# Kernel optimization log

Hardware: AMD Instinct MI355X
Metric: run time of the kernel (lower is better)

Reference implementation:

```python
import jax, jax.numpy as jnp
import numpy as np

N, E, D, H = 50000, 400000, 64, 2  # nodes, edges, model_dim, heads


def setup_inputs() -> dict:
    key = jax.random.key(0)
    ks = jax.random.split(key, 11)
    lim = 1.0 / np.sqrt(D)        # torch Linear default init bound (fan_in = D)
    lim_o = 1.0 / np.sqrt(H * D)  # O has fan_in = H*D under merge='cat'
    u = lambda k, shape, l: jax.random.uniform(k, shape, jnp.float32, -l, l)
    return {
        "node_feature": jax.random.normal(ks[0], (N, D), jnp.float32),
        "Wk": u(ks[1], (H, D, D), lim), "bk": u(ks[2], (H, D), lim),
        "Wq": u(ks[3], (H, D, D), lim), "bq": u(ks[4], (H, D), lim),
        "Wv": u(ks[5], (H, D, D), lim), "bv": u(ks[6], (H, D), lim),
        "Wo": u(ks[7], (D, H * D), lim_o), "bo": u(ks[8], (D,), lim_o),
        "src": jax.random.randint(ks[9], (E,), 0, N, jnp.int32),
        "dst": jax.random.randint(ks[10], (E,), 0, N, jnp.int32),
    }


def reference(node_feature, Wk, bk, Wq, bq, Wv, bv, Wo, bo, src, dst):
    # message_func: per-edge gather + per-head K/Q/V linears (torch Linear: x @ W.T + b)
    src_nf = node_feature[src]                               # [E, D]
    dst_nf = node_feature[dst]                               # [E, D]
    k = jnp.einsum('ed,hfd->ehf', src_nf, Wk) + bk           # [E, H, D]
    q = jnp.einsum('ed,hfd->ehf', dst_nf, Wq) + bq           # [E, H, D]
    v = jnp.einsum('ed,hfd->ehf', src_nf, Wv) + bv           # [E, H, D]
    score = jnp.sum(k * q, axis=-1)                          # [E, H]

    # reduce_func: mailbox softmax over incoming edges per dst node (segment softmax)
    m = jax.ops.segment_max(score, dst, num_segments=N)      # [N, H]
    m = jnp.where(jnp.isfinite(m), m, jnp.zeros_like(m))     # nodes with no in-edges
    es = jnp.exp(score - m[dst])                             # [E, H]
    denom = jax.ops.segment_sum(es, dst, num_segments=N)     # [N, H]
    w = es / denom[dst]                                      # [E, H] attention weights
    wv = jax.ops.segment_sum(w[..., None] * v, dst, num_segments=N)  # [N, H, D]

    # apply_nodes: merge='cat' over heads, then O linear; weight = mean over heads
    out_nf = jnp.einsum('nf,of->no', wv.reshape(N, H * D), Wo) + bo  # [N, D]
    edge_weight = w.mean(axis=-1)                            # [E] (per-edge, mean over heads)
    return out_nf, edge_weight
```

## Files before the change

kernel.cpp:

```cpp
#include <hip/hip_runtime.h>
#include <hip/hip_bf16.h>
#include <cstdint>


#define BCAP 32

using short8 = __attribute__((ext_vector_type(8))) short;
using f32x4 = __attribute__((ext_vector_type(4))) float;

__device__ __forceinline__ unsigned short f2bf(float f) {
  __hip_bfloat16 h = __float2bfloat16(f);
  return *reinterpret_cast<unsigned short*>(&h);
}
__device__ __forceinline__ void bf8(const uint4 u, float* f) {
  union { unsigned int i; float v; } a;
  a.i = u.x << 16; f[0] = a.v;  a.i = u.x & 0xffff0000u; f[1] = a.v;
  a.i = u.y << 16; f[2] = a.v;  a.i = u.y & 0xffff0000u; f[3] = a.v;
  a.i = u.z << 16; f[4] = a.v;  a.i = u.z & 0xffff0000u; f[5] = a.v;
  a.i = u.w << 16; f[6] = a.v;  a.i = u.w & 0xffff0000u; f[7] = a.v;
}
__device__ __forceinline__ float dot8(const uint4 a, const uint4 b, float s) {
  float af[8], bfv[8];
  bf8(a, af);
  bf8(b, bfv);
#pragma unroll
  for (int j = 0; j < 8; ++j) s += af[j] * bfv[j];
  return s;
}
__device__ __forceinline__ float gmax16(float v) {
#pragma unroll
  for (int m = 1; m < 16; m <<= 1) v = fmaxf(v, __shfl_xor(v, m, 64));
  return v;
}
__device__ __forceinline__ float gsum16(float v) {
#pragma unroll
  for (int m = 1; m < 16; m <<= 1) v += __shfl_xor(v, m, 64);
  return v;
}

__global__ __launch_bounds__(256) void prep_kernel(
    const float* __restrict__ nf, unsigned short* __restrict__ nfb,
    const float* __restrict__ Wk, const float* __restrict__ Wq,
    const float* __restrict__ Wv, const float* __restrict__ Wo,
    const float* __restrict__ bq, const float* __restrict__ bv,
    const float* __restrict__ bo,
    unsigned short* __restrict__ Mb, unsigned short* __restrict__ Fb,
    float* __restrict__ qb, float* __restrict__ fbias,
    const int* __restrict__ src, const int* __restrict__ dst,
    int* __restrict__ cnt, int2* __restrict__ bucket,
    int nf_f4, int E, int SB, int FB) {
  if (blockIdx.x < SB) {
    for (int idx = blockIdx.x * 256 + threadIdx.x; idx < 16576; idx += SB * 256) {
      if (idx < 8192) {
        const int hf = idx >> 6, j = idx & 63, h = hf >> 6, f = hf & 63;
        const float* wkp = Wk + h * 4096 + f;
        const float* wqp = Wq + h * 4096 + j;
        float s = 0.f;
        for (int i = 0; i < 64; ++i) s += wkp[i * 64] * wqp[i * 64];
        Mb[idx] = f2bf(s);
      } else if (idx < 16384) {
        const int r = idx - 8192;
        const int o = r >> 7, hj = r & 127, h = hj >> 6, j = hj & 63;
        const float* wop = Wo + o * 128 + h * 64;
        const float* wvp = Wv + h * 4096 + j;
        float s = 0.f;
        for (int i = 0; i < 64; ++i) s += wop[i] * wvp[i * 64];
        Fb[r] = f2bf(s);
      } else if (idx < 16512) {
        const int hf = idx - 16384, h = hf >> 6, f = hf & 63;
        const float* wkp = Wk + h * 4096 + f;
        const float* bqp = bq + h * 64;
        float s = 0.f;
        for (int i = 0; i < 64; ++i) s += wkp[i * 64] * bqp[i];
        qb[hf] = s;
      } else if (idx < 16576) {
        const int o = idx - 16512;
        float s = bo[o];
        for (int hi = 0; hi < 128; ++hi) s += Wo[o * 128 + hi] * bv[hi];
        fbias[o] = s;
      }
    }
    return;
  }
  if (blockIdx.x < SB + FB) {
    for (int i = (blockIdx.x - SB) * 256 + threadIdx.x; i < nf_f4; i += FB * 256) {
      const float4 x = ((const float4*)nf)[i];
      uint2 p;
      p.x = (unsigned)f2bf(x.x) | ((unsigned)f2bf(x.y) << 16);
      p.y = (unsigned)f2bf(x.z) | ((unsigned)f2bf(x.w) << 16);
      ((uint2*)nfb)[i] = p;
    }
    return;
  }
  const int CB = gridDim.x - SB - FB;
  for (int e = (blockIdx.x - SB - FB) * 256 + threadIdx.x; e < E; e += CB * 256) {
    const int d = dst[e];
    const int pos = atomicAdd(&cnt[d], 1);
    if (pos < BCAP) bucket[(size_t)d * BCAP + pos] = make_int2(e, src[e]);
  }
}

__global__ __launch_bounds__(256) void node_kernel(
    const unsigned short* __restrict__ nfb,
    const unsigned short* __restrict__ Mb, const float* __restrict__ qb,
    const int2* __restrict__ bucket, const int* __restrict__ cnt,
    const unsigned short* __restrict__ Fb, const float* __restrict__ fbias,
    const float* __restrict__ bo,
    float* __restrict__ out, float* __restrict__ eout, int N) {
  __shared__ uint4 sqt[16][16];
  __shared__ uint4 swv[16][16];

  const int lane = threadIdx.x & 63;
  const int wid = threadIdx.x >> 6;
  const int col = lane & 15;
  const int kslot = lane >> 4;
  const int k0 = kslot * 8;
  const int base = blockIdx.x * 16;

  {
    const int bnode = min(base + col, N - 1);
    const unsigned short* np = nfb + (size_t)bnode * 64;
    const short8 xb0 = *(const short8*)(np + k0);
    const short8 xb1 = *(const short8*)(np + 32 + k0);
#pragma unroll
    for (int tt = 0; tt < 2; ++tt) {
      const int t8 = wid * 2 + tt;
      const unsigned short* mp = Mb + (size_t)(t8 * 16 + col) * 64;
      const short8 fa0 = *(const short8*)(mp + k0);
      const short8 fa1 = *(const short8*)(mp + 32 + k0);
      f32x4 acc = {0.f, 0.f, 0.f, 0.f};
      acc = __builtin_amdgcn_mfma_f32_16x16x32_bf16(fa0, xb0, acc, 0, 0, 0);
      acc = __builtin_amdgcn_mfma_f32_16x16x32_bf16(fa1, xb1, acc, 0, 0, 0);
      const int hf = t8 * 16 + kslot * 4;
      const float4 bias = *(const float4*)(qb + hf);
      uint2 p;
      p.x = (unsigned)f2bf(acc[0] + bias.x) | ((unsigned)f2bf(acc[1] + bias.y) << 16);
      p.y = (unsigned)f2bf(acc[2] + bias.z) | ((unsigned)f2bf(acc[3] + bias.w) << 16);
      const int c4 = hf >> 3;
      const int sub = (hf >> 2) & 1;
      ((uint2*)&sqt[col][c4 ^ col])[sub] = p;
    }
  }
  __syncthreads();

  const int sl = lane & 15;
  const int g16 = lane & 48;
  const int c8 = sl & 7;
  const int nl = wid * 4 + (lane >> 4);
  const int node = base + nl;
  const bool valid = node < N;
  const int nodeq = valid ? node : N - 1;
  const int deg = valid ? min(cnt[node], BCAP) : 0;

  int wdeg = deg;
  wdeg = max(wdeg, __shfl_xor(wdeg, 16, 64));
  wdeg = max(wdeg, __shfl_xor(wdeg, 32, 64));
  wdeg = __builtin_amdgcn_readfirstlane(wdeg);

  const uint4 qt = sqt[nl][sl ^ nl];

  uint4 packed = make_uint4(0u, 0u, 0u, 0u);

  if (wdeg <= 16) {
    int2 es = make_int2(0, 0);
    if (sl < deg) es = bucket[(size_t)nodeq * BCAP + sl];
    const int e_my = es.x;
    const int s_my = (sl < deg) ? es.y : 0;

    int s_i[16];
#pragma unroll
    for (int i = 0; i < 16; ++i) s_i[i] = __shfl(s_my, g16 + i, 64);

    uint4 x_i[16];
#pragma unroll
    for (int i = 0; i < 16; ++i)
      x_i[i] = *(const uint4*)(nfb + (size_t)s_i[i] * 64 + c8 * 8);

    float sc0 = -1e30f, sc1 = -1e30f;
#pragma unroll
    for (int i = 0; i < 16; ++i) {
      float p = dot8(x_i[i], qt, 0.f);
#pragma unroll
      for (int m = 1; m < 8; m <<= 1) p += __shfl_xor(p, m, 64);
      const float other = __shfl_xor(p, 8, 64);
      const float t0 = (sl < 8) ? p : other;
      const float t1 = (sl < 8) ? other : p;
      if (sl == i) { sc0 = t0; sc1 = t1; }
    }
    if (sl >= deg) { sc0 = -1e30f; sc1 = -1e30f; }

    const float m0 = gmax16(sc0);
    const float m1 = gmax16(sc1);
    const float w0 = __expf(sc0 - m0);
    const float w1 = __expf(sc1 - m1);
    const float den0 = gsum16(w0);
    const float den1 = gsum16(w1);
    if (sl < deg) eout[e_my] = 0.5f * (w0 / den0 + w1 / den1);

    float agg[8];
#pragma unroll
    for (int j = 0; j < 8; ++j) agg[j] = 0.f;
#pragma unroll
    for (int i = 0; i < 16; ++i) {
      const float wi0 = __shfl(w0, g16 + i, 64);
      const float wi1 = __shfl(w1, g16 + i, 64);
      float xf[8];
      bf8(x_i[i], xf);
      const float ws = (sl < 8) ? wi0 : wi1;
#pragma unroll
      for (int j = 0; j < 8; ++j) agg[j] += ws * xf[j];
    }
    const float dinv = (deg == 0) ? 0.f : ((sl < 8) ? 1.f / den0 : 1.f / den1);
    unsigned short ob[8];
#pragma unroll
    for (int j = 0; j < 8; ++j) ob[j] = f2bf(agg[j] * dinv);
    packed = *(const uint4*)ob;
  } else {
    float m0 = -1e30f, m1 = -1e30f, den0 = 0.f, den1 = 0.f;
    float agg[8];
#pragma unroll
    for (int j = 0; j < 8; ++j) agg[j] = 0.f;

    for (int c0 = 0; c0 < deg; c0 += 16) {
      const int cn = min(16, deg - c0);
      int s_my = 0;
      if (sl < cn) s_my = bucket[(size_t)nodeq * BCAP + c0 + sl].y;

      int s_i[16];
#pragma unroll
      for (int i = 0; i < 16; ++i) s_i[i] = __shfl(s_my, g16 + i, 64);
      uint4 x_i[16];
#pragma unroll
      for (int i = 0; i < 16; ++i)
        x_i[i] = *(const uint4*)(nfb + (size_t)s_i[i] * 64 + c8 * 8);

      float sc0 = -1e30f, sc1 = -1e30f;
#pragma unroll
      for (int i = 0; i < 16; ++i) {
        float p = dot8(x_i[i], qt, 0.f);
#pragma unroll
        for (int m = 1; m < 8; m <<= 1) p += __shfl_xor(p, m, 64);
        const float other = __shfl_xor(p, 8, 64);
        const float t0 = (sl < 8) ? p : other;
        const float t1 = (sl < 8) ? other : p;
        if (sl == i) { sc0 = t0; sc1 = t1; }
      }
      if (sl >= cn) { sc0 = -1e30f; sc1 = -1e30f; }

      const float cm0 = gmax16(sc0);
      const float cm1 = gmax16(sc1);
      const float nm0 = fmaxf(m0, cm0), nm1 = fmaxf(m1, cm1);
      const float r0 = __expf(m0 - nm0), r1 = __expf(m1 - nm1);
      den0 *= r0; den1 *= r1;
      const float racc = (sl < 8) ? r0 : r1;
#pragma unroll
      for (int j = 0; j < 8; ++j) agg[j] *= racc;
      m0 = nm0; m1 = nm1;

      const float w0 = __expf(sc0 - m0);
      const float w1 = __expf(sc1 - m1);
      den0 += gsum16(w0);
      den1 += gsum16(w1);

#pragma unroll
      for (int i = 0; i < 16; ++i) {
        const float wi0 = __shfl(w0, g16 + i, 64);
        const float wi1 = __shfl(w1, g16 + i, 64);
        float xf[8];
        bf8(x_i[i], xf);
        const float ws = (sl < 8) ? wi0 : wi1;
#pragma unroll
        for (int j = 0; j < 8; ++j) agg[j] += ws * xf[j];
      }
    }

    const float dinv = (deg == 0) ? 0.f : ((sl < 8) ? 1.f / den0 : 1.f / den1);
    unsigned short ob[8];
#pragma unroll
    for (int j = 0; j < 8; ++j) ob[j] = f2bf(agg[j] * dinv);
    packed = *(const uint4*)ob;

    for (int i = 0; i < deg; ++i) {
      const int2 es = bucket[(size_t)nodeq * BCAP + i];
      const uint4 xv = *(const uint4*)(nfb + (size_t)es.y * 64 + c8 * 8);
      float p = dot8(xv, qt, 0.f);
#pragma unroll
      for (int m = 1; m < 8; m <<= 1) p += __shfl_xor(p, m, 64);
      const float other = __shfl_xor(p, 8, 64);
      const float t0 = (sl < 8) ? p : other;
      const float t1 = (sl < 8) ? other : p;
      if (sl == 0)
        eout[es.x] = 0.5f * (__expf(t0 - m0) / den0 + __expf(t1 - m1) / den1);
    }
  }

  swv[nl][sl ^ nl] = packed;
  __syncthreads();

  const int hi = lane >> 4;
  short8 fa[4];
#pragma unroll
  for (int c = 0; c < 4; ++c)
    fa[c] = *(const short8*)&swv[col][(c * 4 + hi) ^ col];

  const int o = wid * 16 + col;
  const unsigned short* bp = Fb + (size_t)o * 128;
  f32x4 acco = {0.f, 0.f, 0.f, 0.f};
#pragma unroll
  for (int c = 0; c < 4; ++c) {
    const short8 fbb = *(const short8*)(bp + c * 32 + hi * 8);
    acco = __builtin_amdgcn_mfma_f32_16x16x32_bf16(fa[c], fbb, acco, 0, 0, 0);
  }
  const float fb_o = fbias[o];
  const float bo_o = bo[o];
#pragma unroll
  for (int r = 0; r < 4; ++r) {
    const int nrow = base + hi * 4 + r;
    if (nrow < N) {
      const float bias = (cnt[nrow] > 0) ? fb_o : bo_o;
      out[(size_t)nrow * 64 + o] = acco[r] + bias;
    }
  }
}

extern "C" void kernel_launch(void* const* d_in, const int* in_sizes, int n_in,
                              void* d_out, int out_size, void* d_ws, size_t ws_size,
                              hipStream_t stream) {
  const float* nf = (const float*)d_in[0];
  const float* Wk = (const float*)d_in[1];
  const float* Wq = (const float*)d_in[3];
  const float* bq = (const float*)d_in[4];
  const float* Wv = (const float*)d_in[5];
  const float* bv = (const float*)d_in[6];
  const float* Wo = (const float*)d_in[7];
  const float* bo = (const float*)d_in[8];
  const int* src = (const int*)d_in[9];
  const int* dst = (const int*)d_in[10];

  const int N = in_sizes[0] / 64;
  const int E = in_sizes[9];

  float* out_nf = (float*)d_out;
  float* eout = (float*)d_out + (size_t)N * 64;

  char* w = (char*)d_ws;
  auto alloc = [&](size_t bytes) -> void* {
    void* p = (void*)w;
    w += (bytes + 255) / 256 * 256;
    return p;
  };
  unsigned short* nfb = (unsigned short*)alloc((size_t)N * 64 * 2);
  unsigned short* Mb = (unsigned short*)alloc((size_t)128 * 64 * 2);
  unsigned short* Fb = (unsigned short*)alloc((size_t)64 * 128 * 2);
  float* qb = (float*)alloc(128 * 4);
  float* fbias = (float*)alloc(64 * 4);
  int* cnt = (int*)alloc((size_t)N * 4);
  int2* bucket = (int2*)alloc((size_t)N * BCAP * 8);

  const int SB = 16;
  const int FB = 128;
  const int CB = 256;
  const int nf_f4 = (N * 64) / 4;

  hipMemsetAsync(cnt, 0, (size_t)N * 4, stream);

  prep_kernel<<<SB + FB + CB, 256, 0, stream>>>(
      nf, nfb, Wk, Wq, Wv, Wo, bq, bv, bo, Mb, Fb, qb, fbias, src, dst, cnt,
      bucket, nf_f4, E, SB, FB);
  node_kernel<<<(N + 15) / 16, 256, 0, stream>>>(nfb, Mb, qb, bucket, cnt, Fb,
                                                 fbias, bo, out_nf, eout, N);
}
```

Measured before the change: 98.94 us.

## Make each wave own 16 nodes independently, removing block-level barriers

Each wave now handles its own 16-node tile end to end. It computes the full 8-tile Q projection for its nodes and loops over 4 rounds of 4 nodes for the segment softmax and aggregation. It then runs the output projection on its own tile, so __syncthreads is no longer needed and the grid shrinks by a factor of 4. The shared-memory tiles get per-wave slices padded to 17 in place of XOR swizzling. In exchange each wave does 4x the projection MFMA work and walks its nodes serially, which gives less latency hiding per wave and could raise register pressure.

```diff
diff --git a/kernel.cpp b/kernel.cpp
--- a/kernel.cpp
+++ b/kernel.cpp
@@ -107,24 +107,24 @@
     const unsigned short* __restrict__ Fb, const float* __restrict__ fbias,
     const float* __restrict__ bo,
     float* __restrict__ out, float* __restrict__ eout, int N) {
-  __shared__ uint4 sqt[16][16];
-  __shared__ uint4 swv[16][16];
+  __shared__ uint4 sqt[4][16][17];
+  __shared__ uint4 swv[4][16][17];
 
   const int lane = threadIdx.x & 63;
   const int wid = threadIdx.x >> 6;
   const int col = lane & 15;
   const int kslot = lane >> 4;
   const int k0 = kslot * 8;
-  const int base = blockIdx.x * 16;
+  const int blockW = blockIdx.x * 64 + wid * 16;
+  if (blockW >= N) return;
 
   {
-    const int bnode = min(base + col, N - 1);
+    const int bnode = min(blockW + col, N - 1);
     const unsigned short* np = nfb + (size_t)bnode * 64;
     const short8 xb0 = *(const short8*)(np + k0);
     const short8 xb1 = *(const short8*)(np + 32 + k0);
 #pragma unroll
-    for (int tt = 0; tt < 2; ++tt) {
-      const int t8 = wid * 2 + tt;
+    for (int t8 = 0; t8 < 8; ++t8) {
       const unsigned short* mp = Mb + (size_t)(t8 * 16 + col) * 64;
       const short8 fa0 = *(const short8*)(mp + k0);
       const short8 fa1 = *(const short8*)(mp + 32 + k0);
@@ -136,99 +136,43 @@
       uint2 p;
       p.x = (unsigned)f2bf(acc[0] + bias.x) | ((unsigned)f2bf(acc[1] + bias.y) << 16);
       p.y = (unsigned)f2bf(acc[2] + bias.z) | ((unsigned)f2bf(acc[3] + bias.w) << 16);
-      const int c4 = hf >> 3;
-      const int sub = (hf >> 2) & 1;
-      ((uint2*)&sqt[col][c4 ^ col])[sub] = p;
-    }
-  }
-  __syncthreads();
+      const int c4 = t8 * 2 + (kslot >> 1);
+      const int sub = kslot & 1;
+      ((uint2*)&sqt[wid][col][c4])[sub] = p;
+    }
+  }
 
   const int sl = lane & 15;
   const int g16 = lane & 48;
+  const int g = lane >> 4;
   const int c8 = sl & 7;
-  const int nl = wid * 4 + (lane >> 4);
-  const int node = base + nl;
-  const bool valid = node < N;
-  const int nodeq = valid ? node : N - 1;
-  const int deg = valid ? min(cnt[node], BCAP) : 0;
-
-  int wdeg = deg;
-  wdeg = max(wdeg, __shfl_xor(wdeg, 16, 64));
-  wdeg = max(wdeg, __shfl_xor(wdeg, 32, 64));
-  wdeg = __builtin_amdgcn_readfirstlane(wdeg);
-
-  const uint4 qt = sqt[nl][sl ^ nl];
-
-  uint4 packed = make_uint4(0u, 0u, 0u, 0u);
-
-  if (wdeg <= 16) {
-    int2 es = make_int2(0, 0);
-    if (sl < deg) es = bucket[(size_t)nodeq * BCAP + sl];
-    const int e_my = es.x;
-    const int s_my = (sl < deg) ? es.y : 0;
-
-    int s_i[16];
-#pragma unroll
-    for (int i = 0; i < 16; ++i) s_i[i] = __shfl(s_my, g16 + i, 64);
-
-    uint4 x_i[16];
-#pragma unroll
-    for (int i = 0; i < 16; ++i)
-      x_i[i] = *(const uint4*)(nfb + (size_t)s_i[i] * 64 + c8 * 8);
-
-    float sc0 = -1e30f, sc1 = -1e30f;
-#pragma unroll
-    for (int i = 0; i < 16; ++i) {
-      float p = dot8(x_i[i], qt, 0.f);
-#pragma unroll
-      for (int m = 1; m < 8; m <<= 1) p += __shfl_xor(p, m, 64);
-      const float other = __shfl_xor(p, 8, 64);
-      const float t0 = (sl < 8) ? p : other;
-      const float t1 = (sl < 8) ? other : p;
-      if (sl == i) { sc0 = t0; sc1 = t1; }
-    }
-    if (sl >= deg) { sc0 = -1e30f; sc1 = -1e30f; }
-
-    const float m0 = gmax16(sc0);
-    const float m1 = gmax16(sc1);
-    const float w0 = __expf(sc0 - m0);
-    const float w1 = __expf(sc1 - m1);
-    const float den0 = gsum16(w0);
-    const float den1 = gsum16(w1);
-    if (sl < deg) eout[e_my] = 0.5f * (w0 / den0 + w1 / den1);
-
-    float agg[8];
-#pragma unroll
-    for (int j = 0; j < 8; ++j) agg[j] = 0.f;
-#pragma unroll
-    for (int i = 0; i < 16; ++i) {
-      const float wi0 = __shfl(w0, g16 + i, 64);
-      const float wi1 = __shfl(w1, g16 + i, 64);
-      float xf[8];
-      bf8(x_i[i], xf);
-      const float ws = (sl < 8) ? wi0 : wi1;
-#pragma unroll
-      for (int j = 0; j < 8; ++j) agg[j] += ws * xf[j];
-    }
-    const float dinv = (deg == 0) ? 0.f : ((sl < 8) ? 1.f / den0 : 1.f / den1);
-    unsigned short ob[8];
-#pragma unroll
-    for (int j = 0; j < 8; ++j) ob[j] = f2bf(agg[j] * dinv);
-    packed = *(const uint4*)ob;
-  } else {
-    float m0 = -1e30f, m1 = -1e30f, den0 = 0.f, den1 = 0.f;
-    float agg[8];
-#pragma unroll
-    for (int j = 0; j < 8; ++j) agg[j] = 0.f;
-
-    for (int c0 = 0; c0 < deg; c0 += 16) {
-      const int cn = min(16, deg - c0);
-      int s_my = 0;
-      if (sl < cn) s_my = bucket[(size_t)nodeq * BCAP + c0 + sl].y;
+
+#pragma unroll 1
+  for (int r = 0; r < 4; ++r) {
+    const int nl = r * 4 + g;
+    const int node = blockW + nl;
+    const bool valid = node < N;
+    const int nodeq = valid ? node : N - 1;
+    const int deg = valid ? min(cnt[node], BCAP) : 0;
+
+    int rdeg = deg;
+    rdeg = max(rdeg, __shfl_xor(rdeg, 16, 64));
+    rdeg = max(rdeg, __shfl_xor(rdeg, 32, 64));
+    rdeg = __builtin_amdgcn_readfirstlane(rdeg);
+
+    uint4 packed = make_uint4(0u, 0u, 0u, 0u);
+    const uint4 qt = sqt[wid][nl][sl];
+
+    if (rdeg <= 16) {
+      int2 es = make_int2(0, 0);
+      if (sl < deg) es = bucket[(size_t)nodeq * BCAP + sl];
+      const int e_my = es.x;
+      const int s_my = (sl < deg) ? es.y : 0;
 
       int s_i[16];
 #pragma unroll
       for (int i = 0; i < 16; ++i) s_i[i] = __shfl(s_my, g16 + i, 64);
+
       uint4 x_i[16];
 #pragma unroll
       for (int i = 0; i < 16; ++i)
@@ -245,23 +189,19 @@
         const float t1 = (sl < 8) ? other : p;
         if (sl == i) { sc0 = t0; sc1 = t1; }
       }
-      if (sl >= cn) { sc0 = -1e30f; sc1 = -1e30f; }
-
-      const float cm0 = gmax16(sc0);
-      const float cm1 = gmax16(sc1);
-      const float nm0 = fmaxf(m0, cm0), nm1 = fmaxf(m1, cm1);
-      const float r0 = __expf(m0 - nm0), r1 = __expf(m1 - nm1);
-      den0 *= r0; den1 *= r1;
-      const float racc = (sl < 8) ? r0 : r1;
-#pragma unroll
-      for (int j = 0; j < 8; ++j) agg[j] *= racc;
-      m0 = nm0; m1 = nm1;
-
+      if (sl >= deg) { sc0 = -1e30f; sc1 = -1e30f; }
+
+      const float m0 = gmax16(sc0);
+      const float m1 = gmax16(sc1);
       const float w0 = __expf(sc0 - m0);
       const float w1 = __expf(sc1 - m1);
-      den0 += gsum16(w0);
-      den1 += gsum16(w1);
-
+      const float den0 = gsum16(w0);
+      const float den1 = gsum16(w1);
+      if (sl < deg) eout[e_my] = 0.5f * (w0 / den0 + w1 / den1);
+
+      float agg[8];
+#pragma unroll
+      for (int j = 0; j < 8; ++j) agg[j] = 0.f;
 #pragma unroll
       for (int i = 0; i < 16; ++i) {
         const float wi0 = __shfl(w0, g16 + i, 64);
@@ -272,53 +212,112 @@
 #pragma unroll
         for (int j = 0; j < 8; ++j) agg[j] += ws * xf[j];
       }
-    }
-
-    const float dinv = (deg == 0) ? 0.f : ((sl < 8) ? 1.f / den0 : 1.f / den1);
-    unsigned short ob[8];
-#pragma unroll
-    for (int j = 0; j < 8; ++j) ob[j] = f2bf(agg[j] * dinv);
-    packed = *(const uint4*)ob;
-
-    for (int i = 0; i < deg; ++i) {
-      const int2 es = bucket[(size_t)nodeq * BCAP + i];
-      const uint4 xv = *(const uint4*)(nfb + (size_t)es.y * 64 + c8 * 8);
-      float p = dot8(xv, qt, 0.f);
-#pragma unroll
-      for (int m = 1; m < 8; m <<= 1) p += __shfl_xor(p, m, 64);
-      const float other = __shfl_xor(p, 8, 64);
-      const float t0 = (sl < 8) ? p : other;
-      const float t1 = (sl < 8) ? other : p;
-      if (sl == 0)
-        eout[es.x] = 0.5f * (__expf(t0 - m0) / den0 + __expf(t1 - m1) / den1);
-    }
-  }
-
-  swv[nl][sl ^ nl] = packed;
-  __syncthreads();
-
-  const int hi = lane >> 4;
-  short8 fa[4];
-#pragma unroll
-  for (int c = 0; c < 4; ++c)
-    fa[c] = *(const short8*)&swv[col][(c * 4 + hi) ^ col];
-
-  const int o = wid * 16 + col;
-  const unsigned short* bp = Fb + (size_t)o * 128;
-  f32x4 acco = {0.f, 0.f, 0.f, 0.f};
-#pragma unroll
-  for (int c = 0; c < 4; ++c) {
-    const short8 fbb = *(const short8*)(bp + c * 32 + hi * 8);
-    acco = __builtin_amdgcn_mfma_f32_16x16x32_bf16(fa[c], fbb, acco, 0, 0, 0);
-  }
-  const float fb_o = fbias[o];
-  const float bo_o = bo[o];
-#pragma unroll
-  for (int r = 0; r < 4; ++r) {
-    const int nrow = base + hi * 4 + r;
-    if (nrow < N) {
-      const float bias = (cnt[nrow] > 0) ? fb_o : bo_o;
-      out[(size_t)nrow * 64 + o] = acco[r] + bias;
+      const float dinv = (deg == 0) ? 0.f : ((sl < 8) ? 1.f / den0 : 1.f / den1);
+      unsigned short ob[8];
+#pragma unroll
+      for (int j = 0; j < 8; ++j) ob[j] = f2bf(agg[j] * dinv);
+      packed = *(const uint4*)ob;
+    } else {
+      float m0 = -1e30f, m1 = -1e30f, den0 = 0.f, den1 = 0.f;
+      float agg[8];
+#pragma unroll
+      for (int j = 0; j < 8; ++j) agg[j] = 0.f;
+
+      for (int c0 = 0; c0 < deg; c0 += 16) {
+        const int cn = min(16, deg - c0);
+        int s_my = 0;
+        if (sl < cn) s_my = bucket[(size_t)nodeq * BCAP + c0 + sl].y;
+
+        int s_i[16];
+#pragma unroll
+        for (int i = 0; i < 16; ++i) s_i[i] = __shfl(s_my, g16 + i, 64);
+        uint4 x_i[16];
+#pragma unroll
+        for (int i = 0; i < 16; ++i)
+          x_i[i] = *(const uint4*)(nfb + (size_t)s_i[i] * 64 + c8 * 8);
+
+        float sc0 = -1e30f, sc1 = -1e30f;
+#pragma unroll
+        for (int i = 0; i < 16; ++i) {
+          float p = dot8(x_i[i], qt, 0.f);
+#pragma unroll
+          for (int m = 1; m < 8; m <<= 1) p += __shfl_xor(p, m, 64);
+          const float other = __shfl_xor(p, 8, 64);
+          const float t0 = (sl < 8) ? p : other;
+          const float t1 = (sl < 8) ? other : p;
+          if (sl == i) { sc0 = t0; sc1 = t1; }
+        }
+        if (sl >= cn) { sc0 = -1e30f; sc1 = -1e30f; }
+
+        const float cm0 = gmax16(sc0);
+        const float cm1 = gmax16(sc1);
+        const float nm0 = fmaxf(m0, cm0), nm1 = fmaxf(m1, cm1);
+        const float r0 = __expf(m0 - nm0), r1 = __expf(m1 - nm1);
+        den0 *= r0; den1 *= r1;
+        const float racc = (sl < 8) ? r0 : r1;
+#pragma unroll
+        for (int j = 0; j < 8; ++j) agg[j] *= racc;
+        m0 = nm0; m1 = nm1;
+
+        const float w0 = __expf(sc0 - m0);
+        const float w1 = __expf(sc1 - m1);
+        den0 += gsum16(w0);
+        den1 += gsum16(w1);
+
+#pragma unroll
+        for (int i = 0; i < 16; ++i) {
+          const float wi0 = __shfl(w0, g16 + i, 64);
+          const float wi1 = __shfl(w1, g16 + i, 64);
+          float xf[8];
+          bf8(x_i[i], xf);
+          const float ws = (sl < 8) ? wi0 : wi1;
+#pragma unroll
+          for (int j = 0; j < 8; ++j) agg[j] += ws * xf[j];
+        }
+      }
+
+      const float dinv = (deg == 0) ? 0.f : ((sl < 8) ? 1.f / den0 : 1.f / den1);
+      unsigned short ob[8];
+#pragma unroll
+      for (int j = 0; j < 8; ++j) ob[j] = f2bf(agg[j] * dinv);
+      packed = *(const uint4*)ob;
+
+      for (int i = 0; i < deg; ++i) {
+        const int2 es = bucket[(size_t)nodeq * BCAP + i];
+        const uint4 xv = *(const uint4*)(nfb + (size_t)es.y * 64 + c8 * 8);
+        float p = dot8(xv, qt, 0.f);
+#pragma unroll
+        for (int m = 1; m < 8; m <<= 1) p += __shfl_xor(p, m, 64);
+        const float other = __shfl_xor(p, 8, 64);
+        const float t0 = (sl < 8) ? p : other;
+        const float t1 = (sl < 8) ? other : p;
+        if (sl == 0)
+          eout[es.x] = 0.5f * (__expf(t0 - m0) / den0 + __expf(t1 - m1) / den1);
+      }
+    }
+
+    swv[wid][nl][sl] = packed;
+  }
+
+  const int degcol = (blockW + col < N) ? cnt[blockW + col] : 1;
+#pragma unroll
+  for (int t = 0; t < 4; ++t) {
+    f32x4 acco = {0.f, 0.f, 0.f, 0.f};
+#pragma unroll
+    for (int c = 0; c < 4; ++c) {
+      const short8 fa =
+          *(const short8*)(Fb + (size_t)(t * 16 + col) * 128 + c * 32 + k0);
+      const short8 fb = *(const short8*)&swv[wid][col][c * 4 + kslot];
+      acco = __builtin_amdgcn_mfma_f32_16x16x32_bf16(fa, fb, acco, 0, 0, 0);
+    }
+#pragma unroll
+    for (int rr = 0; rr < 4; ++rr) {
+      const int o = t * 16 + kslot * 4 + rr;
+      const int nrow = blockW + col;
+      if (nrow < N) {
+        const float bias = (degcol > 0) ? fbias[o] : bo[o];
+        out[(size_t)nrow * 64 + o] = acco[rr] + bias;
+      }
     }
   }
 }
@@ -367,6 +366,6 @@
   prep_kernel<<<SB + FB + CB, 256, 0, stream>>>(
       nf, nfb, Wk, Wq, Wv, Wo, bq, bv, bo, Mb, Fb, qb, fbias, src, dst, cnt,
       bucket, nf_f4, E, SB, FB);
-  node_kernel<<<(N + 15) / 16, 256, 0, stream>>>(nfb, Mb, qb, bucket, cnt, Fb,
+  node_kernel<<<(N + 63) / 64, 256, 0, stream>>>(nfb, Mb, qb, bucket, cnt, Fb,
                                                  fbias, bo, out_nf, eout, N);
 }
```

Result: slower. 103.2 us (+4.3%).

## Issue bucket and neighbor gathers before the Q-projection barrier; rebalance prep grid

Applied to the files above, without the earlier changes.

Moves the per-node degree and bucket loads, along with the 16 neighbor-feature gathers for the low-degree path, ahead of the MFMA Q-projection and its __syncthreads. The gather latency can then overlap the projection work instead of starting after the barrier. The bucket load is now unconditional, with the source index clamped into range, so reads of unfilled slots stay safe. It also replaces the repeated divisions with precomputed reciprocals and enlarges the prep kernel's feature-conversion and counting block groups, at the cost of more registers held live across the barrier.

```diff
diff --git a/kernel.cpp b/kernel.cpp
--- a/kernel.cpp
+++ b/kernel.cpp
@@ -117,6 +117,19 @@
   const int k0 = kslot * 8;
   const int base = blockIdx.x * 16;
 
+  const int sl = col;
+  const int g16 = lane & 48;
+  const int c8 = sl & 7;
+  const int nl = wid * 4 + kslot;
+  const int node = base + nl;
+  const bool valid = node < N;
+  const int nodeq = valid ? node : N - 1;
+
+  const int deg = valid ? min(cnt[node], BCAP) : 0;
+  const int2 es = bucket[(size_t)nodeq * BCAP + sl];
+  const int e_my = es.x;
+  const int s_my = min(max(es.y, 0), N - 1);
+
   {
     const int bnode = min(base + col, N - 1);
     const unsigned short* np = nfb + (size_t)bnode * 64;
@@ -141,41 +154,28 @@
       ((uint2*)&sqt[col][c4 ^ col])[sub] = p;
     }
   }
-  __syncthreads();
-
-  const int sl = lane & 15;
-  const int g16 = lane & 48;
-  const int c8 = sl & 7;
-  const int nl = wid * 4 + (lane >> 4);
-  const int node = base + nl;
-  const bool valid = node < N;
-  const int nodeq = valid ? node : N - 1;
-  const int deg = valid ? min(cnt[node], BCAP) : 0;
 
   int wdeg = deg;
   wdeg = max(wdeg, __shfl_xor(wdeg, 16, 64));
   wdeg = max(wdeg, __shfl_xor(wdeg, 32, 64));
   wdeg = __builtin_amdgcn_readfirstlane(wdeg);
 
-  const uint4 qt = sqt[nl][sl ^ nl];
-
-  uint4 packed = make_uint4(0u, 0u, 0u, 0u);
-
+  uint4 x_i[16];
   if (wdeg <= 16) {
-    int2 es = make_int2(0, 0);
-    if (sl < deg) es = bucket[(size_t)nodeq * BCAP + sl];
-    const int e_my = es.x;
-    const int s_my = (sl < deg) ? es.y : 0;
-
     int s_i[16];
 #pragma unroll
     for (int i = 0; i < 16; ++i) s_i[i] = __shfl(s_my, g16 + i, 64);
-
-    uint4 x_i[16];
 #pragma unroll
     for (int i = 0; i < 16; ++i)
       x_i[i] = *(const uint4*)(nfb + (size_t)s_i[i] * 64 + c8 * 8);
-
+  }
+
+  __syncthreads();
+
+  const uint4 qt = sqt[nl][sl ^ nl];
+  uint4 packed = make_uint4(0u, 0u, 0u, 0u);
+
+  if (wdeg <= 16) {
     float sc0 = -1e30f, sc1 = -1e30f;
 #pragma unroll
     for (int i = 0; i < 16; ++i) {
@@ -195,7 +195,9 @@
     const float w1 = __expf(sc1 - m1);
     const float den0 = gsum16(w0);
     const float den1 = gsum16(w1);
-    if (sl < deg) eout[e_my] = 0.5f * (w0 / den0 + w1 / den1);
+    const float i0 = 1.f / den0;
+    const float i1 = 1.f / den1;
+    if (sl < deg) eout[e_my] = 0.5f * (w0 * i0 + w1 * i1);
 
     float agg[8];
 #pragma unroll
@@ -210,7 +212,7 @@
 #pragma unroll
       for (int j = 0; j < 8; ++j) agg[j] += ws * xf[j];
     }
-    const float dinv = (deg == 0) ? 0.f : ((sl < 8) ? 1.f / den0 : 1.f / den1);
+    const float dinv = (deg == 0) ? 0.f : ((sl < 8) ? i0 : i1);
     unsigned short ob[8];
 #pragma unroll
     for (int j = 0; j < 8; ++j) ob[j] = f2bf(agg[j] * dinv);
@@ -223,21 +225,21 @@
 
     for (int c0 = 0; c0 < deg; c0 += 16) {
       const int cn = min(16, deg - c0);
-      int s_my = 0;
-      if (sl < cn) s_my = bucket[(size_t)nodeq * BCAP + c0 + sl].y;
+      int s_c = 0;
+      if (sl < cn) s_c = bucket[(size_t)nodeq * BCAP + c0 + sl].y;
 
       int s_i[16];
 #pragma unroll
-      for (int i = 0; i < 16; ++i) s_i[i] = __shfl(s_my, g16 + i, 64);
-      uint4 x_i[16];
+      for (int i = 0; i < 16; ++i) s_i[i] = __shfl(s_c, g16 + i, 64);
+      uint4 xc[16];
 #pragma unroll
       for (int i = 0; i < 16; ++i)
-        x_i[i] = *(const uint4*)(nfb + (size_t)s_i[i] * 64 + c8 * 8);
+        xc[i] = *(const uint4*)(nfb + (size_t)s_i[i] * 64 + c8 * 8);
 
       float sc0 = -1e30f, sc1 = -1e30f;
 #pragma unroll
       for (int i = 0; i < 16; ++i) {
-        float p = dot8(x_i[i], qt, 0.f);
+        float p = dot8(xc[i], qt, 0.f);
 #pragma unroll
         for (int m = 1; m < 8; m <<= 1) p += __shfl_xor(p, m, 64);
         const float other = __shfl_xor(p, 8, 64);
@@ -267,7 +269,7 @@
         const float wi0 = __shfl(w0, g16 + i, 64);
         const float wi1 = __shfl(w1, g16 + i, 64);
         float xf[8];
-        bf8(x_i[i], xf);
+        bf8(xc[i], xf);
         const float ws = (sl < 8) ? wi0 : wi1;
 #pragma unroll
         for (int j = 0; j < 8; ++j) agg[j] += ws * xf[j];
@@ -281,8 +283,8 @@
     packed = *(const uint4*)ob;
 
     for (int i = 0; i < deg; ++i) {
-      const int2 es = bucket[(size_t)nodeq * BCAP + i];
-      const uint4 xv = *(const uint4*)(nfb + (size_t)es.y * 64 + c8 * 8);
+      const int2 e2 = bucket[(size_t)nodeq * BCAP + i];
+      const uint4 xv = *(const uint4*)(nfb + (size_t)e2.y * 64 + c8 * 8);
       float p = dot8(xv, qt, 0.f);
 #pragma unroll
       for (int m = 1; m < 8; m <<= 1) p += __shfl_xor(p, m, 64);
@@ -290,7 +292,7 @@
       const float t0 = (sl < 8) ? p : other;
       const float t1 = (sl < 8) ? other : p;
       if (sl == 0)
-        eout[es.x] = 0.5f * (__expf(t0 - m0) / den0 + __expf(t1 - m1) / den1);
+        eout[e2.x] = 0.5f * (__expf(t0 - m0) / den0 + __expf(t1 - m1) / den1);
     }
   }
 
@@ -358,8 +360,8 @@
   int2* bucket = (int2*)alloc((size_t)N * BCAP * 8);
 
   const int SB = 16;
-  const int FB = 128;
-  const int CB = 256;
+  const int FB = 384;
+  const int CB = 368;
   const int nf_f4 = (N * 64) / 4;
 
   hipMemsetAsync(cnt, 0, (size_t)N * 4, stream);
```

Result: slower. 137.7 us (+39.1%).
